# Optimization experiments

Hardware: AMD Instinct MI355X
Metric: run time of the kernel (lower is better)

Reference implementation:

```python
import jax, jax.numpy as jnp
from jax import lax
import numpy as np

B, P, G, C = 16, 6000, 128, 10
PC_MIN = np.array([-54.0, -54.0, -5.0], np.float32)
PC_MAX = np.array([54.0, 54.0, 3.0], np.float32)
CENTER_RADIUS = 1.5
CANDIDATE_TOPK = 5
NUM_HEADS = 6
CLS_W, ALPHA, GAMMA = 2.0, 0.25, 2.0
REG_W, IOU_W = 0.25, 0.25
EPS = 1e-12
INF1, INF2 = 10000.0, 100000.0


def _aabb(boxes):
    # boxes: (N,7) [cx,cy,cz,dx,dy,dz,yaw] -> AABB (min,max) of the 8 rotated corners
    c, d, yaw = boxes[:, :3], boxes[:, 3:6], boxes[:, 6]
    ca, sa = jnp.abs(jnp.cos(yaw)), jnp.abs(jnp.sin(yaw))
    hx = 0.5 * (d[:, 0] * ca + d[:, 1] * sa)
    hy = 0.5 * (d[:, 0] * sa + d[:, 1] * ca)
    h = jnp.stack([hx, hy, 0.5 * d[:, 2]], -1)
    return c - h, c + h


def _iou3d(pred7, gt7):
    # axis-aligned 3D IoU over corner AABBs (reference stand-in for rotated BboxOverlaps3D)
    pmin, pmax = _aabb(pred7)
    gmin, gmax = _aabb(gt7)
    lo = jnp.maximum(pmin[:, None], gmin[None])   # (P,G,3)
    hi = jnp.minimum(pmax[:, None], gmax[None])
    inter = jnp.prod(jnp.maximum(hi - lo, 0.0), -1)
    vp = jnp.prod(pmax - pmin, -1)
    vg = jnp.prod(gmax - gmin, -1)
    return inter / (vp[:, None] + vg[None] - inter + 1e-7)


def _cost_matrix(pred_logits, pred_boxes, gt_boxes, gt_labels):
    # --- focal classification cost ---
    p = jax.nn.sigmoid(pred_logits)                                  # (P,C)
    neg = -jnp.log(1.0 - p + EPS) * (1.0 - ALPHA) * p ** GAMMA
    pos = -jnp.log(p + EPS) * ALPHA * (1.0 - p) ** GAMMA
    cls_cost = (pos - neg)[:, gt_labels] * CLS_W                     # (P,G)

    gt_norm = jnp.concatenate([gt_boxes[:, :3], jnp.log(gt_boxes[:, 3:6]),
                               jnp.sin(gt_boxes[:, 6:7]), jnp.cos(gt_boxes[:, 6:7])], -1)  # (G,8)
    reg_cost = jnp.abs(pred_boxes[:, None, :8] - gt_norm[None]).sum(-1) * REG_W

    # --- IoU cost on denormalized pred boxes ---
    yaw = jnp.arctan2(pred_boxes[:, 6], pred_boxes[:, 7])
    pred7 = jnp.concatenate([pred_boxes[:, :3], jnp.exp(pred_boxes[:, 3:6]), yaw[:, None]], -1)
    ious = _iou3d(pred7, gt_boxes)                                   # (P,G)
    iou_cost = -ious * IOU_W

    # --- in-gt-box / in-center geometric prior ---
    ctr = pred_boxes[:, :3]
    gmin, gmax = _aabb(gt_boxes)
    in_box = jnp.all((ctr[:, None] > gmin[None]) & (ctr[:, None] < gmax[None]), -1)  # (P,G)
    gc, gd = gt_boxes[:, :3], gt_boxes[:, 3:6]
    lo = gc - CENTER_RADIUS * gd
    hi = gc + CENTER_RADIUS * gd
    in_ctr = jnp.all((ctr[:, None] > lo[None]) & (ctr[:, None] < hi[None]), -1)
    valid = jnp.any(in_box, 1) | jnp.any(in_ctr, 1)                  # (P,)
    in_both = in_box & in_ctr

    cost = cls_cost + reg_cost + iou_cost + (~in_both).astype(cls_cost.dtype) * 100.0
    cost = cost + (~valid).astype(cls_cost.dtype)[:, None] * INF1
    return cost, ious, valid


def _assign(pred_logits, pred_boxes, gt_boxes, gt_labels, head_idx):
    cost, ious, valid = _cost_matrix(pred_logits, pred_boxes, gt_boxes, gt_labels)

    # dynamic-k per gt: sum of top-k ious minus head-schedule offset, truncated, min 1
    k = min(CANDIDATE_TOPK, P)
    topk_ious = lax.top_k(ious.T, k)[0]                              # (G,k)
    dyn = jnp.maximum((topk_ious.sum(1) - 0.5 * (NUM_HEADS - head_idx)).astype(jnp.int32), 1)

    # per-gt lowest-cost top-dyn selection via double argsort ranks
    ranks = jnp.argsort(jnp.argsort(cost, axis=0), axis=0)           # (P,G)
    matching = (ranks < dyn[None, :]).astype(cost.dtype)

    # priors matched to >1 gt: keep only the min-cost gt
    prior_mask = matching.sum(1) > 1
    onehot_min = jax.nn.one_hot(jnp.argmin(cost, 1), G, dtype=cost.dtype)
    matching = jnp.where(prior_mask[:, None], onehot_min, matching)

    rows = jnp.arange(P)

    def cond(s):
        i, cst, m = s
        return jnp.any(m.sum(0) == 0) & (i < G + 8)

    def body(s):
        i, cst, m = s
        cst = cst + (m.sum(1) > 0).astype(cst.dtype)[:, None] * INF2
        unmatched = m.sum(0) == 0                                    # (G,)
        pos = jnp.argmin(cst, 0)                                     # (G,) best prior per gt
        m = jnp.where((rows[:, None] == pos[None]) & unmatched[None], 1.0, m)
        over = jnp.any(m.sum(1) > 1)
        oh = jax.nn.one_hot(jnp.argmin(cst, 1), G, dtype=cst.dtype)
        m = jnp.where(over & prior_mask[:, None], oh, m)             # stale mask, as in torch source
        return i + 1, cst, m

    _, _, matching = lax.while_loop(cond, body, (jnp.int32(0), cost, matching))

    fg = matching.sum(1) > 0                                         # (P,) foreground mask
    matched = jnp.where(fg, jnp.argmax(matching, 1), -1).astype(jnp.int32)
    return fg, matched


def setup_inputs():
    key = jax.random.key(0)
    k1, k2, k3, k4, k5, k6, k7, k8 = jax.random.split(key, 8)
    pred_logits = jax.random.normal(k1, (B, P, C), jnp.float32)
    ctr = jax.random.uniform(k2, (B, P, 3), jnp.float32, jnp.array(PC_MIN), jnp.array(PC_MAX))
    logsz = jnp.log(jax.random.uniform(k3, (B, P, 3), jnp.float32, 1.0, 4.0))
    ang = jax.random.uniform(k4, (B, P, 1), jnp.float32, -np.pi, np.pi)
    vel = jax.random.normal(k5, (B, P, 2), jnp.float32)
    pred_boxes = jnp.concatenate([ctr, logsz, jnp.sin(ang), jnp.cos(ang), vel], -1)
    gctr = jax.random.uniform(k6, (B, G, 3), jnp.float32, jnp.array(PC_MIN), jnp.array(PC_MAX))
    gsz = jax.random.uniform(k7, (B, G, 3), jnp.float32, 1.0, 5.0)
    gyaw = jax.random.uniform(k8, (B, G, 1), jnp.float32, -np.pi, np.pi)
    gt_boxes = jnp.concatenate([gctr, gsz, gyaw], -1)
    gt_labels = jax.random.randint(jax.random.fold_in(key, 99), (B, G), 0, C)
    return {"pred_logits": pred_logits, "pred_boxes": pred_boxes,
            "gt_boxes": gt_boxes, "gt_labels": gt_labels, "head_idx": 5}


def reference(pred_logits, pred_boxes, gt_boxes, gt_labels, head_idx):
    f = lambda pl, pb, gb, gl: _assign(pl, pb, gb, gl, head_idx)
    fg, matched = jax.vmap(f)(pred_logits, pred_boxes, gt_boxes, gt_labels)
    return fg, matched
```

## Files before the change

### kernel.cpp

```cpp
#include <hip/hip_runtime.h>
#include <stdint.h>
#include <math.h>

#define NB 16
#define NP 6000
#define NG 128
#define NC 10
#define CHUNK 24
#define SELMAX 8
#define GSTR 24

static_assert(CHUNK * 256 >= NP, "chunk covers P");

typedef unsigned long long u64;

__device__ __forceinline__ uint32_t fkey(float f) {
  uint32_t u = __float_as_uint(f);
  return (u & 0x80000000u) ? ~u : (u | 0x80000000u);
}
__device__ __forceinline__ float fkey_inv(uint32_t k) {
  uint32_t u = (k & 0x80000000u) ? (k & 0x7fffffffu) : ~k;
  return __uint_as_float(u);
}
__device__ __forceinline__ u64 shfl_xor_u64(u64 v, int m) {
  uint32_t lo = (uint32_t)v, hi = (uint32_t)(v >> 32);
  lo = (uint32_t)__shfl_xor((int)lo, m, 64);
  hi = (uint32_t)__shfl_xor((int)hi, m, 64);
  return ((u64)hi << 32) | lo;
}

__global__ void prep_gt_kernel(const float* __restrict__ gt_boxes,
                               const int* __restrict__ gt_labels,
                               float* __restrict__ gtaux) {
#pragma clang fp contract(off)
  int b = blockIdx.x, g = threadIdx.x;
  if (g >= NG) return;
  const float* gb = gt_boxes + ((size_t)b * NG + g) * 7;
  float cx = gb[0], cy = gb[1], cz = gb[2];
  float dx = gb[3], dy = gb[4], dz = gb[5];
  float yaw = gb[6];
  float cyw = cosf(yaw), syw = sinf(yaw);
  float ca = fabsf(cyw), sa = fabsf(syw);
  float hx = 0.5f * (dx * ca + dy * sa);
  float hy = 0.5f * (dx * sa + dy * ca);
  float hz = 0.5f * dz;
  float gmin0 = cx - hx, gmin1 = cy - hy, gmin2 = cz - hz;
  float gmax0 = cx + hx, gmax1 = cy + hy, gmax2 = cz + hz;
  float vg = ((gmax0 - gmin0) * (gmax1 - gmin1)) * (gmax2 - gmin2);
  float* o = gtaux + ((size_t)b * NG + g) * GSTR;
  o[0] = gmin0; o[1] = gmin1; o[2] = gmin2;
  o[3] = gmax0; o[4] = gmax1; o[5] = gmax2;
  o[6] = cx - 1.5f * dx; o[7] = cy - 1.5f * dy; o[8] = cz - 1.5f * dz;
  o[9] = cx + 1.5f * dx; o[10] = cy + 1.5f * dy; o[11] = cz + 1.5f * dz;
  o[12] = cx; o[13] = cy; o[14] = cz;
  o[15] = logf(dx); o[16] = logf(dy); o[17] = logf(dz);
  o[18] = syw; o[19] = cyw;
  o[20] = vg;
  o[21] = __int_as_float(gt_labels[(size_t)b * NG + g]);
  o[22] = 0.0f; o[23] = 0.0f;
}

__global__ __launch_bounds__(256) void costmat_kernel(
    const float* __restrict__ pred_logits,
    const float* __restrict__ pred_boxes,
    const float* __restrict__ gtaux,
    float* __restrict__ cost,
    float* __restrict__ iouM,
    int* __restrict__ validArr,
    int* __restrict__ rowminArr,
    int* __restrict__ rowcnt,
    int* __restrict__ rowassign) {
#pragma clang fp contract(off)
  __shared__ __align__(16) float shg[NG * GSTR];
  __shared__ float shcls[256 * 11];
  const int b = blockIdx.y, tid = threadIdx.x;
  for (int j = tid; j < NG * GSTR; j += 256)
    shg[j] = gtaux[(size_t)b * NG * GSTR + j];
  const int p = blockIdx.x * 256 + tid;
  const size_t idx = (size_t)b * NP + p;
  if (p < NP) {
    const float* lg = pred_logits + idx * NC;
    for (int c = 0; c < NC; ++c) {
      float x = lg[c];
      float pr = 1.0f / (1.0f + expf(-x));
      float neg = (-logf(1.0f - pr + 1e-12f) * 0.75f) * (pr * pr);
      float pos = (-logf(pr + 1e-12f) * 0.25f) * ((1.0f - pr) * (1.0f - pr));
      shcls[tid * 11 + c] = (pos - neg) * 2.0f;
    }
  }
  __syncthreads();
  if (p >= NP) return;

  const float* bx = pred_boxes + idx * 10;
  float b0 = bx[0], b1 = bx[1], b2 = bx[2], b3 = bx[3], b4 = bx[4];
  float b5 = bx[5], b6 = bx[6], b7 = bx[7];
  float yaw = atan2f(b6, b7);
  float d0 = expf(b3), d1 = expf(b4), d2 = expf(b5);
  float ca = fabsf(cosf(yaw)), sa = fabsf(sinf(yaw));
  float hx = 0.5f * (d0 * ca + d1 * sa);
  float hy = 0.5f * (d0 * sa + d1 * ca);
  float hz = 0.5f * d2;
  float pmin0 = b0 - hx, pmin1 = b1 - hy, pmin2 = b2 - hz;
  float pmax0 = b0 + hx, pmax1 = b1 + hy, pmax2 = b2 + hz;
  float vp = ((pmax0 - pmin0) * (pmax1 - pmin1)) * (pmax2 - pmin2);

  int valid = 0;
  float best = INFINITY;
  int bg = 0;
  size_t cidx = (size_t)b * NG * NP + p;
  for (int g = 0; g < NG; ++g) {
    const float* s = &shg[g * GSTR];
    float4 q0 = *(const float4*)(s + 0);
    float4 q1 = *(const float4*)(s + 4);
    float4 q2 = *(const float4*)(s + 8);
    float4 q3 = *(const float4*)(s + 12);
    float4 q4 = *(const float4*)(s + 16);
    float2 q5 = *(const float2*)(s + 20);
    float gmin0 = q0.x, gmin1 = q0.y, gmin2 = q0.z;
    float gmax0 = q0.w, gmax1 = q1.x, gmax2 = q1.y;
    float lo0 = q1.z, lo1 = q1.w, lo2 = q2.x;
    float hi0 = q2.y, hi1 = q2.z, hi2 = q2.w;
    int label = __float_as_int(q5.y);
    float cls = shcls[tid * 11 + label];
    float r = fabsf(b0 - q3.x);
    r = r + fabsf(b1 - q3.y);
    r = r + fabsf(b2 - q3.z);
    r = r + fabsf(b3 - q3.w);
    r = r + fabsf(b4 - q4.x);
    r = r + fabsf(b5 - q4.y);
    r = r + fabsf(b6 - q4.z);
    r = r + fabsf(b7 - q4.w);
    float reg = r * 0.25f;
    float li0 = fmaxf(pmin0, gmin0), li1 = fmaxf(pmin1, gmin1), li2 = fmaxf(pmin2, gmin2);
    float hj0 = fminf(pmax0, gmax0), hj1 = fminf(pmax1, gmax1), hj2 = fminf(pmax2, gmax2);
    float e0 = fmaxf(hj0 - li0, 0.0f), e1 = fmaxf(hj1 - li1, 0.0f), e2 = fmaxf(hj2 - li2, 0.0f);
    float inter = (e0 * e1) * e2;
    float iou = inter / (((vp + q5.x) - inter) + 1e-7f);
    bool inb = (b0 > gmin0) && (b0 < gmax0) && (b1 > gmin1) &&
               (b1 < gmax1) && (b2 > gmin2) && (b2 < gmax2);
    bool inc = (b0 > lo0) && (b0 < hi0) && (b1 > lo1) && (b1 < hi1) &&
               (b2 > lo2) && (b2 < hi2);
    float cc = ((cls + reg) + (-(iou * 0.25f))) + ((inb && inc) ? 0.0f : 100.0f);
    cost[cidx] = cc;
    iouM[cidx] = iou;
    cidx += NP;
    valid |= (int)(inb || inc);
    if (cc < best) { best = cc; bg = g; }
  }
  validArr[idx] = valid;
  rowminArr[idx] = bg;
  rowcnt[idx] = 0;
  rowassign[idx] = 0x7fffffff;
}

__global__ __launch_bounds__(256) void select_kernel(
    const float* __restrict__ cost,
    const float* __restrict__ iouM,
    const int* __restrict__ validArr,
    const int* __restrict__ head_ptr,
    int* __restrict__ colsel,
    int* __restrict__ rowcnt,
    int* __restrict__ rowassign) {
#pragma clang fp contract(off)
  const int g = blockIdx.x, b = blockIdx.y, tid = threadIdx.x;
  const int lane = tid & 63, wid = tid >> 6;
  const size_t cbase = ((size_t)(b * NG + g)) * NP;
  const size_t rowbase = (size_t)b * NP;
  float lc[CHUNK], li[CHUNK];
#pragma unroll
  for (int i = 0; i < CHUNK; ++i) {
    int p = i * 256 + tid;
    if (p < NP) {
      lc[i] = cost[cbase + p] + (validArr[rowbase + p] ? 0.0f : 10000.0f);
      li[i] = iouM[cbase + p];
    } else {
      lc[i] = INFINITY;
      li[i] = -INFINITY;
    }
  }
  __shared__ u64 sred[4];
  __shared__ float s_t5[5];
  __shared__ int s_dyn;
  __shared__ int s_sel[SELMAX];

  for (int k = 0; k < 5; ++k) {
    u64 best = 0;
#pragma unroll
    for (int i = 0; i < CHUNK; ++i) {
      u64 key = ((u64)fkey(li[i]) << 32) | (unsigned)(i * 256 + tid);
      if (key > best) best = key;
    }
#pragma unroll
    for (int o = 1; o < 64; o <<= 1) {
      u64 t = shfl_xor_u64(best, o);
      if (t > best) best = t;
    }
    __syncthreads();
    if (lane == 0) sred[wid] = best;
    __syncthreads();
    u64 r = sred[0];
    if (sred[1] > r) r = sred[1];
    if (sred[2] > r) r = sred[2];
    if (sred[3] > r) r = sred[3];
    if (tid == 0) s_t5[k] = fkey_inv((uint32_t)(r >> 32));
    int d = (int)(r & 0xffffffffu) - tid;
    if (d >= 0 && (d & 255) == 0) { int ii = d >> 8; if (ii < CHUNK) li[ii] = -INFINITY; }
  }
  __syncthreads();
  if (tid == 0) {
    float s = (((s_t5[0] + s_t5[1]) + s_t5[2]) + s_t5[3]) + s_t5[4];
    float adj = s - 0.5f * (float)(6 - head_ptr[0]);
    int dyn = (int)adj;
    if (dyn < 1) dyn = 1;
    if (dyn > SELMAX) dyn = SELMAX;
    s_dyn = dyn;
  }
  __syncthreads();
  const int dyn = s_dyn;

  for (int k = 0; k < dyn; ++k) {
    u64 best = ~0ull;
#pragma unroll
    for (int i = 0; i < CHUNK; ++i) {
      u64 key = ((u64)fkey(lc[i]) << 32) | (unsigned)(i * 256 + tid);
      if (key < best) best = key;
    }
#pragma unroll
    for (int o = 1; o < 64; o <<= 1) {
      u64 t = shfl_xor_u64(best, o);
      if (t < best) best = t;
    }
    __syncthreads();
    if (lane == 0) sred[wid] = best;
    __syncthreads();
    u64 r = sred[0];
    if (sred[1] < r) r = sred[1];
    if (sred[2] < r) r = sred[2];
    if (sred[3] < r) r = sred[3];
    int pw = (int)(r & 0xffffffffu);
    if (tid == 0) s_sel[k] = pw;
    int d = pw - tid;
    if (d >= 0 && (d & 255) == 0) { int ii = d >> 8; if (ii < CHUNK) lc[ii] = INFINITY; }
  }
  __syncthreads();
  if (tid == 0) {
    for (int k = 0; k < SELMAX; ++k) {
      int s = (k < dyn) ? s_sel[k] : -1;
      colsel[((size_t)(b * NG + g)) * SELMAX + k] = s;
      if (s >= 0) {
        atomicAdd(&rowcnt[rowbase + s], 1);
        atomicMin(&rowassign[rowbase + s], g);
      }
    }
  }
}

__global__ void colcnt_a_kernel(const int* __restrict__ colsel,
                                const int* __restrict__ rowcnt,
                                int* __restrict__ colcnt) {
  int i = blockIdx.x * 256 + threadIdx.x;
  if (i >= NB * NG) return;
  int b = i / NG;
  int cnt = 0;
  for (int k = 0; k < SELMAX; ++k) {
    int s = colsel[(size_t)i * SELMAX + k];
    if (s >= 0 && rowcnt[(size_t)b * NP + s] == 1) cnt++;
  }
  colcnt[i] = cnt;
}

__global__ void colcnt_b_kernel(const int* __restrict__ rowcnt,
                                const int* __restrict__ rowmin,
                                int* __restrict__ colcnt) {
  int b = blockIdx.y, p = blockIdx.x * 256 + threadIdx.x;
  if (p >= NP) return;
  size_t idx = (size_t)b * NP + p;
  if (rowcnt[idx] > 1) atomicAdd(&colcnt[b * NG + rowmin[idx]], 1);
}

__global__ __launch_bounds__(256) void fixup_kernel(const float* __restrict__ cost,
                                                    const int* __restrict__ colcnt,
                                                    const int* __restrict__ rowcnt,
                                                    const int* __restrict__ validArr,
                                                    int* __restrict__ rowassign) {
#pragma clang fp contract(off)
  const int g = blockIdx.x, b = blockIdx.y, tid = threadIdx.x;
  if (colcnt[b * NG + g] != 0) return;
  const size_t cbase = ((size_t)(b * NG + g)) * NP;
  const size_t rowbase = (size_t)b * NP;
  u64 best = ~0ull;
  for (int p = tid; p < NP; p += 256) {
    if (rowcnt[rowbase + p] == 0) {
      float c = cost[cbase + p] + (validArr[rowbase + p] ? 0.0f : 10000.0f);
      u64 key = ((u64)fkey(c) << 32) | (unsigned)p;
      if (key < best) best = key;
    }
  }
  __shared__ u64 red[256];
  red[tid] = best;
  __syncthreads();
  for (int offr = 128; offr > 0; offr >>= 1) {
    if (tid < offr) { if (red[tid + offr] < red[tid]) red[tid] = red[tid + offr]; }
    __syncthreads();
  }
  if (tid == 0) {
    int pos = (int)(red[0] & 0xffffffffu);
    atomicMin(&rowassign[rowbase + pos], g);
  }
}

__global__ void output_kernel(const int* __restrict__ rowcnt,
                              const int* __restrict__ rowassign,
                              const int* __restrict__ rowmin,
                              int* __restrict__ out) {
  int b = blockIdx.y, p = blockIdx.x * 256 + threadIdx.x;
  if (p >= NP) return;
  size_t idx = (size_t)b * NP + p;
  int rc = rowcnt[idx];
  int fg, m;
  if (rc == 0) {
    int ra = rowassign[idx];
    if (ra == 0x7fffffff) { fg = 0; m = -1; }
    else { fg = 1; m = ra; }
  } else if (rc == 1) {
    fg = 1; m = rowassign[idx];
  } else {
    fg = 1; m = rowmin[idx];
  }
  out[idx] = fg;
  out[(size_t)NB * NP + idx] = m;
}

extern "C" void kernel_launch(void* const* d_in, const int* in_sizes, int n_in,
                              void* d_out, int out_size, void* d_ws, size_t ws_size,
                              hipStream_t stream) {
  const float* pred_logits = (const float*)d_in[0];
  const float* pred_boxes = (const float*)d_in[1];
  const float* gt_boxes = (const float*)d_in[2];
  const int* gt_labels = (const int*)d_in[3];
  const int* head = (const int*)d_in[4];
  (void)in_sizes; (void)n_in; (void)out_size; (void)ws_size;

  char* w = (char*)d_ws;
  size_t off = 0;
  auto alloc = [&](size_t bytes) -> void* {
    void* p = w + off;
    off += (bytes + 255) & ~(size_t)255;
    return p;
  };
  float* cost = (float*)alloc((size_t)NB * NG * NP * 4);
  float* iouM = (float*)alloc((size_t)NB * NG * NP * 4);
  float* gtaux = (float*)alloc((size_t)NB * NG * GSTR * 4);
  int* validArr = (int*)alloc((size_t)NB * NP * 4);
  int* colsel = (int*)alloc((size_t)NB * NG * SELMAX * 4);
  int* rowcnt = (int*)alloc((size_t)NB * NP * 4);
  int* rowassign = (int*)alloc((size_t)NB * NP * 4);
  int* rowmin = (int*)alloc((size_t)NB * NP * 4);
  int* colcnt = (int*)alloc((size_t)NB * NG * 4);

  int* out = (int*)d_out;
  dim3 blk(256);
  prep_gt_kernel<<<dim3(NB), dim3(128), 0, stream>>>(gt_boxes, gt_labels, gtaux);
  costmat_kernel<<<dim3((NP + 255) / 256, NB), blk, 0, stream>>>(
      pred_logits, pred_boxes, gtaux, cost, iouM, validArr, rowmin, rowcnt, rowassign);
  select_kernel<<<dim3(NG, NB), blk, 0, stream>>>(
      cost, iouM, validArr, head, colsel, rowcnt, rowassign);
  colcnt_a_kernel<<<dim3((NB * NG + 255) / 256), blk, 0, stream>>>(colsel, rowcnt, colcnt);
  colcnt_b_kernel<<<dim3((NP + 255) / 256, NB), blk, 0, stream>>>(rowcnt, rowmin, colcnt);
  fixup_kernel<<<dim3(NG, NB), blk, 0, stream>>>(cost, colcnt, rowcnt, validArr, rowassign);
  output_kernel<<<dim3((NP + 255) / 256, NB), blk, 0, stream>>>(rowcnt, rowassign, rowmin, out);
}
```

Measured before the change: 122.4 us.

## Recompute cost on the fly instead of materializing cost and IoU matrices

The full B×G×P cost and IoU matrices are no longer written to global memory. A per-prediction prep kernel stores box auxiliaries and transposed class costs, and the select kernel recomputes costs for two GT columns per block. It keeps a per-thread top-5 of IoU so the top-5 sum needs only five block reductions. Row-minimum and fixup costs are recomputed only for rows that need them. This removes roughly 100 MB of matrix traffic in exchange for extra arithmetic, more registers per thread, and an XCD-aware block-to-batch mapping.

```diff
diff --git a/kernel.cpp b/kernel.cpp
--- a/kernel.cpp
+++ b/kernel.cpp
@@ -9,10 +9,12 @@
 #define CHUNK 24
 #define SELMAX 8
 #define GSTR 24
+#define GCOLS 2
 
 static_assert(CHUNK * 256 >= NP, "chunk covers P");
 
 typedef unsigned long long u64;
+#define NBPs ((size_t)NB * NP)
 
 __device__ __forceinline__ uint32_t fkey(float f) {
   uint32_t u = __float_as_uint(f);
@@ -60,37 +62,33 @@
   o[22] = 0.0f; o[23] = 0.0f;
 }
 
-__global__ __launch_bounds__(256) void costmat_kernel(
+__global__ __launch_bounds__(256) void prep_pred_kernel(
     const float* __restrict__ pred_logits,
     const float* __restrict__ pred_boxes,
     const float* __restrict__ gtaux,
-    float* __restrict__ cost,
-    float* __restrict__ iouM,
-    int* __restrict__ validArr,
-    int* __restrict__ rowminArr,
+    float* __restrict__ paux,
+    float* __restrict__ clst,
     int* __restrict__ rowcnt,
     int* __restrict__ rowassign) {
 #pragma clang fp contract(off)
-  __shared__ __align__(16) float shg[NG * GSTR];
-  __shared__ float shcls[256 * 11];
+  __shared__ float shg[NG * 12];
   const int b = blockIdx.y, tid = threadIdx.x;
-  for (int j = tid; j < NG * GSTR; j += 256)
-    shg[j] = gtaux[(size_t)b * NG * GSTR + j];
+  for (int j = tid; j < NG * 12; j += 256) {
+    int g = j / 12, k = j % 12;
+    shg[j] = gtaux[((size_t)b * NG + g) * GSTR + k];
+  }
+  __syncthreads();
   const int p = blockIdx.x * 256 + tid;
+  if (p >= NP) return;
   const size_t idx = (size_t)b * NP + p;
-  if (p < NP) {
-    const float* lg = pred_logits + idx * NC;
-    for (int c = 0; c < NC; ++c) {
-      float x = lg[c];
-      float pr = 1.0f / (1.0f + expf(-x));
-      float neg = (-logf(1.0f - pr + 1e-12f) * 0.75f) * (pr * pr);
-      float pos = (-logf(pr + 1e-12f) * 0.25f) * ((1.0f - pr) * (1.0f - pr));
-      shcls[tid * 11 + c] = (pos - neg) * 2.0f;
-    }
-  }
-  __syncthreads();
-  if (p >= NP) return;
-
+  const float* lg = pred_logits + idx * NC;
+  for (int c = 0; c < NC; ++c) {
+    float x = lg[c];
+    float pr = 1.0f / (1.0f + expf(-x));
+    float neg = (-logf(1.0f - pr + 1e-12f) * 0.75f) * (pr * pr);
+    float pos = (-logf(pr + 1e-12f) * 0.25f) * ((1.0f - pr) * (1.0f - pr));
+    clst[(size_t)c * NBPs + idx] = (pos - neg) * 2.0f;
+  }
   const float* bx = pred_boxes + idx * 10;
   float b0 = bx[0], b1 = bx[1], b2 = bx[2], b3 = bx[3], b4 = bx[4];
   float b5 = bx[5], b6 = bx[6], b7 = bx[7];
@@ -103,153 +101,217 @@
   float pmin0 = b0 - hx, pmin1 = b1 - hy, pmin2 = b2 - hz;
   float pmax0 = b0 + hx, pmax1 = b1 + hy, pmax2 = b2 + hz;
   float vp = ((pmax0 - pmin0) * (pmax1 - pmin1)) * (pmax2 - pmin2);
-
   int valid = 0;
-  float best = INFINITY;
-  int bg = 0;
-  size_t cidx = (size_t)b * NG * NP + p;
   for (int g = 0; g < NG; ++g) {
-    const float* s = &shg[g * GSTR];
-    float4 q0 = *(const float4*)(s + 0);
-    float4 q1 = *(const float4*)(s + 4);
-    float4 q2 = *(const float4*)(s + 8);
-    float4 q3 = *(const float4*)(s + 12);
-    float4 q4 = *(const float4*)(s + 16);
-    float2 q5 = *(const float2*)(s + 20);
-    float gmin0 = q0.x, gmin1 = q0.y, gmin2 = q0.z;
-    float gmax0 = q0.w, gmax1 = q1.x, gmax2 = q1.y;
-    float lo0 = q1.z, lo1 = q1.w, lo2 = q2.x;
-    float hi0 = q2.y, hi1 = q2.z, hi2 = q2.w;
-    int label = __float_as_int(q5.y);
-    float cls = shcls[tid * 11 + label];
-    float r = fabsf(b0 - q3.x);
-    r = r + fabsf(b1 - q3.y);
-    r = r + fabsf(b2 - q3.z);
-    r = r + fabsf(b3 - q3.w);
-    r = r + fabsf(b4 - q4.x);
-    r = r + fabsf(b5 - q4.y);
-    r = r + fabsf(b6 - q4.z);
-    r = r + fabsf(b7 - q4.w);
-    float reg = r * 0.25f;
-    float li0 = fmaxf(pmin0, gmin0), li1 = fmaxf(pmin1, gmin1), li2 = fmaxf(pmin2, gmin2);
-    float hj0 = fminf(pmax0, gmax0), hj1 = fminf(pmax1, gmax1), hj2 = fminf(pmax2, gmax2);
-    float e0 = fmaxf(hj0 - li0, 0.0f), e1 = fmaxf(hj1 - li1, 0.0f), e2 = fmaxf(hj2 - li2, 0.0f);
-    float inter = (e0 * e1) * e2;
-    float iou = inter / (((vp + q5.x) - inter) + 1e-7f);
-    bool inb = (b0 > gmin0) && (b0 < gmax0) && (b1 > gmin1) &&
-               (b1 < gmax1) && (b2 > gmin2) && (b2 < gmax2);
-    bool inc = (b0 > lo0) && (b0 < hi0) && (b1 > lo1) && (b1 < hi1) &&
-               (b2 > lo2) && (b2 < hi2);
-    float cc = ((cls + reg) + (-(iou * 0.25f))) + ((inb && inc) ? 0.0f : 100.0f);
-    cost[cidx] = cc;
-    iouM[cidx] = iou;
-    cidx += NP;
-    valid |= (int)(inb || inc);
-    if (cc < best) { best = cc; bg = g; }
-  }
-  validArr[idx] = valid;
-  rowminArr[idx] = bg;
+    const float* s = &shg[g * 12];
+    bool inb = (b0 > s[0]) && (b0 < s[3]) && (b1 > s[1]) && (b1 < s[4]) &&
+               (b2 > s[2]) && (b2 < s[5]);
+    bool inc = (b0 > s[6]) && (b0 < s[9]) && (b1 > s[7]) && (b1 < s[10]) &&
+               (b2 > s[8]) && (b2 < s[11]);
+    if (inb || inc) { valid = 1; break; }
+  }
+  float* o = paux + idx * 16;
+  o[0] = b0; o[1] = b1; o[2] = b2; o[3] = b3;
+  o[4] = b4; o[5] = b5; o[6] = b6; o[7] = b7;
+  o[8] = pmin0; o[9] = pmin1; o[10] = pmin2;
+  o[11] = pmax0; o[12] = pmax1; o[13] = pmax2;
+  o[14] = vp; o[15] = valid ? 0.0f : 10000.0f;
   rowcnt[idx] = 0;
   rowassign[idx] = 0x7fffffff;
 }
 
-__global__ __launch_bounds__(256) void select_kernel(
-    const float* __restrict__ cost,
-    const float* __restrict__ iouM,
-    const int* __restrict__ validArr,
+struct GTp {
+  float gmin0, gmin1, gmin2, gmax0, gmax1, gmax2;
+  float lo0, lo1, lo2, hi0, hi1, hi2;
+  float gtn0, gtn1, gtn2, gtn3, gtn4, gtn5, gtn6, gtn7;
+  float vg;
+  int label;
+};
+__device__ __forceinline__ GTp load_gt(const float* __restrict__ gtaux,
+                                       int b, int g) {
+  const float* ga = gtaux + ((size_t)b * NG + g) * GSTR;
+  GTp t;
+  t.gmin0 = ga[0]; t.gmin1 = ga[1]; t.gmin2 = ga[2];
+  t.gmax0 = ga[3]; t.gmax1 = ga[4]; t.gmax2 = ga[5];
+  t.lo0 = ga[6]; t.lo1 = ga[7]; t.lo2 = ga[8];
+  t.hi0 = ga[9]; t.hi1 = ga[10]; t.hi2 = ga[11];
+  t.gtn0 = ga[12]; t.gtn1 = ga[13]; t.gtn2 = ga[14]; t.gtn3 = ga[15];
+  t.gtn4 = ga[16]; t.gtn5 = ga[17]; t.gtn6 = ga[18]; t.gtn7 = ga[19];
+  t.vg = ga[20];
+  t.label = __float_as_int(ga[21]);
+  return t;
+}
+
+__device__ __forceinline__ float cost_base(
+    float b0, float b1, float b2, float b3, float b4, float b5, float b6,
+    float b7, float pmin0, float pmin1, float pmin2, float pmax0, float pmax1,
+    float pmax2, float vp, float cls, const GTp& t, float* iou_out) {
+#pragma clang fp contract(off)
+  float r = fabsf(b0 - t.gtn0);
+  r = r + fabsf(b1 - t.gtn1);
+  r = r + fabsf(b2 - t.gtn2);
+  r = r + fabsf(b3 - t.gtn3);
+  r = r + fabsf(b4 - t.gtn4);
+  r = r + fabsf(b5 - t.gtn5);
+  r = r + fabsf(b6 - t.gtn6);
+  r = r + fabsf(b7 - t.gtn7);
+  float reg = r * 0.25f;
+  float li0 = fmaxf(pmin0, t.gmin0), li1 = fmaxf(pmin1, t.gmin1),
+        li2 = fmaxf(pmin2, t.gmin2);
+  float hj0 = fminf(pmax0, t.gmax0), hj1 = fminf(pmax1, t.gmax1),
+        hj2 = fminf(pmax2, t.gmax2);
+  float e0 = fmaxf(hj0 - li0, 0.0f), e1 = fmaxf(hj1 - li1, 0.0f),
+        e2 = fmaxf(hj2 - li2, 0.0f);
+  float inter = (e0 * e1) * e2;
+  float iou = inter / (((vp + t.vg) - inter) + 1e-7f);
+  bool inb = (b0 > t.gmin0) && (b0 < t.gmax0) && (b1 > t.gmin1) &&
+             (b1 < t.gmax1) && (b2 > t.gmin2) && (b2 < t.gmax2);
+  bool inc = (b0 > t.lo0) && (b0 < t.hi0) && (b1 > t.lo1) && (b1 < t.hi1) &&
+             (b2 > t.lo2) && (b2 < t.hi2);
+  *iou_out = iou;
+  return ((cls + reg) + (-(iou * 0.25f))) + ((inb && inc) ? 0.0f : 100.0f);
+}
+
+__global__ __launch_bounds__(256) void fused_select_kernel(
+    const float* __restrict__ paux,
+    const float* __restrict__ clst,
+    const float* __restrict__ gtaux,
     const int* __restrict__ head_ptr,
     int* __restrict__ colsel,
     int* __restrict__ rowcnt,
     int* __restrict__ rowassign) {
 #pragma clang fp contract(off)
-  const int g = blockIdx.x, b = blockIdx.y, tid = threadIdx.x;
-  const int lane = tid & 63, wid = tid >> 6;
-  const size_t cbase = ((size_t)(b * NG + g)) * NP;
+  const int f = blockIdx.x;
+  const int xcd = f & 7;
+  const int j = f >> 3;
+  const int b = xcd * 2 + (j & 1);
+  const int g0 = (j >> 1) * 2;
+  const int tid = threadIdx.x, lane = tid & 63, wid = tid >> 6;
+
+  GTp gt[GCOLS];
+#pragma unroll
+  for (int c = 0; c < GCOLS; ++c) gt[c] = load_gt(gtaux, b, g0 + c);
+
   const size_t rowbase = (size_t)b * NP;
-  float lc[CHUNK], li[CHUNK];
+  float lc[GCOLS][CHUNK];
+  float t5[GCOLS][5];
+#pragma unroll
+  for (int c = 0; c < GCOLS; ++c)
+#pragma unroll
+    for (int q = 0; q < 5; ++q) t5[c][q] = -INFINITY;
+
 #pragma unroll
   for (int i = 0; i < CHUNK; ++i) {
-    int p = i * 256 + tid;
+    const int p = i * 256 + tid;
     if (p < NP) {
-      lc[i] = cost[cbase + p] + (validArr[rowbase + p] ? 0.0f : 10000.0f);
-      li[i] = iouM[cbase + p];
+      const size_t idx = rowbase + p;
+      const float4* pa = (const float4*)(paux + idx * 16);
+      float4 A = pa[0], Bq = pa[1], Cq = pa[2], Dq = pa[3];
+      const float pen = Dq.w;
+#pragma unroll
+      for (int c = 0; c < GCOLS; ++c) {
+        float cls = clst[(size_t)gt[c].label * NBPs + idx];
+        float iou;
+        float cc = cost_base(A.x, A.y, A.z, A.w, Bq.x, Bq.y, Bq.z, Bq.w,
+                             Cq.x, Cq.y, Cq.z, Cq.w, Dq.x, Dq.y, Dq.z,
+                             cls, gt[c], &iou);
+        lc[c][i] = cc + pen;
+        if (iou > t5[c][4]) {
+          t5[c][4] = iou;
+#pragma unroll
+          for (int q = 4; q > 0; --q) {
+            if (t5[c][q] > t5[c][q - 1]) {
+              float tmp = t5[c][q]; t5[c][q] = t5[c][q - 1]; t5[c][q - 1] = tmp;
+            }
+          }
+        }
+      }
     } else {
-      lc[i] = INFINITY;
-      li[i] = -INFINITY;
+#pragma unroll
+      for (int c = 0; c < GCOLS; ++c) lc[c][i] = INFINITY;
     }
   }
+
   __shared__ u64 sred[4];
-  __shared__ float s_t5[5];
-  __shared__ int s_dyn;
-  __shared__ int s_sel[SELMAX];
-
-  for (int k = 0; k < 5; ++k) {
-    u64 best = 0;
-#pragma unroll
-    for (int i = 0; i < CHUNK; ++i) {
-      u64 key = ((u64)fkey(li[i]) << 32) | (unsigned)(i * 256 + tid);
-      if (key > best) best = key;
+  const int hd = head_ptr[0];
+  int sel[GCOLS][SELMAX];
+  int dynv[GCOLS];
+
+#pragma unroll
+  for (int c = 0; c < GCOLS; ++c) {
+    int hp = 0;
+    float sum5 = 0.0f;
+    for (int rround = 0; rround < 5; ++rround) {
+      float cand = -INFINITY;
+#pragma unroll
+      for (int q = 0; q < 5; ++q)
+        if (hp == q) cand = t5[c][q];
+      u64 key = ((u64)fkey(cand) << 32) | (unsigned)tid;
+#pragma unroll
+      for (int o = 1; o < 64; o <<= 1) {
+        u64 t = shfl_xor_u64(key, o);
+        if (t > key) key = t;
+      }
+      __syncthreads();
+      if (lane == 0) sred[wid] = key;
+      __syncthreads();
+      u64 rr = sred[0];
+      if (sred[1] > rr) rr = sred[1];
+      if (sred[2] > rr) rr = sred[2];
+      if (sred[3] > rr) rr = sred[3];
+      float v = fkey_inv((uint32_t)(rr >> 32));
+      sum5 = (rround == 0) ? v : (sum5 + v);
+      if (tid == (int)(rr & 0xffffffffu)) hp++;
     }
-#pragma unroll
-    for (int o = 1; o < 64; o <<= 1) {
-      u64 t = shfl_xor_u64(best, o);
-      if (t > best) best = t;
-    }
-    __syncthreads();
-    if (lane == 0) sred[wid] = best;
-    __syncthreads();
-    u64 r = sred[0];
-    if (sred[1] > r) r = sred[1];
-    if (sred[2] > r) r = sred[2];
-    if (sred[3] > r) r = sred[3];
-    if (tid == 0) s_t5[k] = fkey_inv((uint32_t)(r >> 32));
-    int d = (int)(r & 0xffffffffu) - tid;
-    if (d >= 0 && (d & 255) == 0) { int ii = d >> 8; if (ii < CHUNK) li[ii] = -INFINITY; }
-  }
-  __syncthreads();
-  if (tid == 0) {
-    float s = (((s_t5[0] + s_t5[1]) + s_t5[2]) + s_t5[3]) + s_t5[4];
-    float adj = s - 0.5f * (float)(6 - head_ptr[0]);
+    float adj = sum5 - 0.5f * (float)(6 - hd);
     int dyn = (int)adj;
     if (dyn < 1) dyn = 1;
     if (dyn > SELMAX) dyn = SELMAX;
-    s_dyn = dyn;
-  }
-  __syncthreads();
-  const int dyn = s_dyn;
-
-  for (int k = 0; k < dyn; ++k) {
-    u64 best = ~0ull;
-#pragma unroll
-    for (int i = 0; i < CHUNK; ++i) {
-      u64 key = ((u64)fkey(lc[i]) << 32) | (unsigned)(i * 256 + tid);
-      if (key < best) best = key;
+    dynv[c] = dyn;
+
+    for (int k = 0; k < dyn; ++k) {
+      u64 best = ~0ull;
+#pragma unroll
+      for (int i = 0; i < CHUNK; ++i) {
+        const int p = i * 256 + tid;
+        bool ok = true;
+#pragma unroll
+        for (int q = 0; q < SELMAX; ++q) ok = ok && (q >= k || p != sel[c][q]);
+        if (ok) {
+          u64 key = ((u64)fkey(lc[c][i]) << 32) | (unsigned)p;
+          if (key < best) best = key;
+        }
+      }
+#pragma unroll
+      for (int o = 1; o < 64; o <<= 1) {
+        u64 t = shfl_xor_u64(best, o);
+        if (t < best) best = t;
+      }
+      __syncthreads();
+      if (lane == 0) sred[wid] = best;
+      __syncthreads();
+      u64 rr = sred[0];
+      if (sred[1] < rr) rr = sred[1];
+      if (sred[2] < rr) rr = sred[2];
+      if (sred[3] < rr) rr = sred[3];
+      int pw = (int)(rr & 0xffffffffu);
+#pragma unroll
+      for (int q = 0; q < SELMAX; ++q)
+        if (q == k) sel[c][q] = pw;
     }
-#pragma unroll
-    for (int o = 1; o < 64; o <<= 1) {
-      u64 t = shfl_xor_u64(best, o);
-      if (t < best) best = t;
-    }
-    __syncthreads();
-    if (lane == 0) sred[wid] = best;
-    __syncthreads();
-    u64 r = sred[0];
-    if (sred[1] < r) r = sred[1];
-    if (sred[2] < r) r = sred[2];
-    if (sred[3] < r) r = sred[3];
-    int pw = (int)(r & 0xffffffffu);
-    if (tid == 0) s_sel[k] = pw;
-    int d = pw - tid;
-    if (d >= 0 && (d & 255) == 0) { int ii = d >> 8; if (ii < CHUNK) lc[ii] = INFINITY; }
-  }
-  __syncthreads();
+  }
+
   if (tid == 0) {
-    for (int k = 0; k < SELMAX; ++k) {
-      int s = (k < dyn) ? s_sel[k] : -1;
-      colsel[((size_t)(b * NG + g)) * SELMAX + k] = s;
-      if (s >= 0) {
-        atomicAdd(&rowcnt[rowbase + s], 1);
-        atomicMin(&rowassign[rowbase + s], g);
+#pragma unroll
+    for (int c = 0; c < GCOLS; ++c) {
+      const size_t cb = ((size_t)(b * NG + g0 + c)) * SELMAX;
+      for (int q = 0; q < SELMAX; ++q) {
+        int s = (q < dynv[c]) ? sel[c][q] : -1;
+        colsel[cb + q] = s;
+        if (s >= 0) {
+          atomicAdd(&rowcnt[rowbase + s], 1);
+          atomicMin(&rowassign[rowbase + s], g0 + c);
+        }
       }
     }
   }
@@ -269,30 +331,61 @@
   colcnt[i] = cnt;
 }
 
-__global__ void colcnt_b_kernel(const int* __restrict__ rowcnt,
-                                const int* __restrict__ rowmin,
-                                int* __restrict__ colcnt) {
-  int b = blockIdx.y, p = blockIdx.x * 256 + threadIdx.x;
+__global__ __launch_bounds__(256) void rowmin_prior_kernel(
+    const float* __restrict__ paux,
+    const float* __restrict__ clst,
+    const float* __restrict__ gtaux,
+    const int* __restrict__ rowcnt,
+    int* __restrict__ rowminArr,
+    int* __restrict__ colcnt) {
+#pragma clang fp contract(off)
+  const int b = blockIdx.y, p = blockIdx.x * 256 + threadIdx.x;
   if (p >= NP) return;
-  size_t idx = (size_t)b * NP + p;
-  if (rowcnt[idx] > 1) atomicAdd(&colcnt[b * NG + rowmin[idx]], 1);
-}
-
-__global__ __launch_bounds__(256) void fixup_kernel(const float* __restrict__ cost,
-                                                    const int* __restrict__ colcnt,
-                                                    const int* __restrict__ rowcnt,
-                                                    const int* __restrict__ validArr,
-                                                    int* __restrict__ rowassign) {
+  const size_t idx = (size_t)b * NP + p;
+  if (rowcnt[idx] <= 1) return;
+  const float4* pa = (const float4*)(paux + idx * 16);
+  float4 A = pa[0], Bq = pa[1], Cq = pa[2], Dq = pa[3];
+  const float pen = Dq.w;
+  float best = INFINITY;
+  int bg = 0;
+  for (int g = 0; g < NG; ++g) {
+    GTp t = load_gt(gtaux, b, g);
+    float cls = clst[(size_t)t.label * NBPs + idx];
+    float iou;
+    float cc = cost_base(A.x, A.y, A.z, A.w, Bq.x, Bq.y, Bq.z, Bq.w,
+                         Cq.x, Cq.y, Cq.z, Cq.w, Dq.x, Dq.y, Dq.z,
+                         cls, t, &iou);
+    float cv = cc + pen;
+    if (cv < best) { best = cv; bg = g; }
+  }
+  rowminArr[idx] = bg;
+  atomicAdd(&colcnt[b * NG + bg], 1);
+}
+
+__global__ __launch_bounds__(256) void fixup_kernel(
+    const float* __restrict__ paux,
+    const float* __restrict__ clst,
+    const float* __restrict__ gtaux,
+    const int* __restrict__ colcnt,
+    const int* __restrict__ rowcnt,
+    int* __restrict__ rowassign) {
 #pragma clang fp contract(off)
   const int g = blockIdx.x, b = blockIdx.y, tid = threadIdx.x;
   if (colcnt[b * NG + g] != 0) return;
-  const size_t cbase = ((size_t)(b * NG + g)) * NP;
   const size_t rowbase = (size_t)b * NP;
+  GTp t = load_gt(gtaux, b, g);
   u64 best = ~0ull;
   for (int p = tid; p < NP; p += 256) {
-    if (rowcnt[rowbase + p] == 0) {
-      float c = cost[cbase + p] + (validArr[rowbase + p] ? 0.0f : 10000.0f);
-      u64 key = ((u64)fkey(c) << 32) | (unsigned)p;
+    const size_t idx = rowbase + p;
+    if (rowcnt[idx] == 0) {
+      const float4* pa = (const float4*)(paux + idx * 16);
+      float4 A = pa[0], Bq = pa[1], Cq = pa[2], Dq = pa[3];
+      float cls = clst[(size_t)t.label * NBPs + idx];
+      float iou;
+      float cc = cost_base(A.x, A.y, A.z, A.w, Bq.x, Bq.y, Bq.z, Bq.w,
+                           Cq.x, Cq.y, Cq.z, Cq.w, Dq.x, Dq.y, Dq.z,
+                           cls, t, &iou);
+      u64 key = ((u64)fkey(cc + Dq.w) << 32) | (unsigned)p;
       if (key < best) best = key;
     }
   }
@@ -311,7 +404,7 @@
 
 __global__ void output_kernel(const int* __restrict__ rowcnt,
                               const int* __restrict__ rowassign,
-                              const int* __restrict__ rowmin,
+                              const int* __restrict__ rowminArr,
                               int* __restrict__ out) {
   int b = blockIdx.y, p = blockIdx.x * 256 + threadIdx.x;
   if (p >= NP) return;
@@ -325,7 +418,7 @@
   } else if (rc == 1) {
     fg = 1; m = rowassign[idx];
   } else {
-    fg = 1; m = rowmin[idx];
+    fg = 1; m = rowminArr[idx];
   }
   out[idx] = fg;
   out[(size_t)NB * NP + idx] = m;
@@ -348,25 +441,27 @@
     off += (bytes + 255) & ~(size_t)255;
     return p;
   };
-  float* cost = (float*)alloc((size_t)NB * NG * NP * 4);
-  float* iouM = (float*)alloc((size_t)NB * NG * NP * 4);
+  float* paux = (float*)alloc((size_t)NB * NP * 16 * 4);
+  float* clst = (float*)alloc((size_t)NC * NB * NP * 4);
   float* gtaux = (float*)alloc((size_t)NB * NG * GSTR * 4);
-  int* validArr = (int*)alloc((size_t)NB * NP * 4);
   int* colsel = (int*)alloc((size_t)NB * NG * SELMAX * 4);
   int* rowcnt = (int*)alloc((size_t)NB * NP * 4);
   int* rowassign = (int*)alloc((size_t)NB * NP * 4);
-  int* rowmin = (int*)alloc((size_t)NB * NP * 4);
+  int* rowminArr = (int*)alloc((size_t)NB * NP * 4);
   int* colcnt = (int*)alloc((size_t)NB * NG * 4);
 
   int* out = (int*)d_out;
   dim3 blk(256);
   prep_gt_kernel<<<dim3(NB), dim3(128), 0, stream>>>(gt_boxes, gt_labels, gtaux);
-  costmat_kernel<<<dim3((NP + 255) / 256, NB), blk, 0, stream>>>(
-      pred_logits, pred_boxes, gtaux, cost, iouM, validArr, rowmin, rowcnt, rowassign);
-  select_kernel<<<dim3(NG, NB), blk, 0, stream>>>(
-      cost, iouM, validArr, head, colsel, rowcnt, rowassign);
+  prep_pred_kernel<<<dim3((NP + 255) / 256, NB), blk, 0, stream>>>(
+      pred_logits, pred_boxes, gtaux, paux, clst, rowcnt, rowassign);
+  fused_select_kernel<<<dim3(NB * NG / GCOLS), blk, 0, stream>>>(
+      paux, clst, gtaux, head, colsel, rowcnt, rowassign);
   colcnt_a_kernel<<<dim3((NB * NG + 255) / 256), blk, 0, stream>>>(colsel, rowcnt, colcnt);
-  colcnt_b_kernel<<<dim3((NP + 255) / 256, NB), blk, 0, stream>>>(rowcnt, rowmin, colcnt);
-  fixup_kernel<<<dim3(NG, NB), blk, 0, stream>>>(cost, colcnt, rowcnt, validArr, rowassign);
-  output_kernel<<<dim3((NP + 255) / 256, NB), blk, 0, stream>>>(rowcnt, rowassign, rowmin, out);
-}
+  rowmin_prior_kernel<<<dim3((NP + 255) / 256, NB), blk, 0, stream>>>(
+      paux, clst, gtaux, rowcnt, rowminArr, colcnt);
+  fixup_kernel<<<dim3(NG, NB), blk, 0, stream>>>(
+      paux, clst, gtaux, colcnt, rowcnt, rowassign);
+  output_kernel<<<dim3((NP + 255) / 256, NB), blk, 0, stream>>>(
+      rowcnt, rowassign, rowminArr, out);
+}
```

Result: slower. 254.8 us (+108.1%).
